# Performance work log

Hardware: AMD Instinct MI355X
Metric: run time of the kernel (lower is better)

The kernel has to match this reference:

```python
import jax, jax.numpy as jnp
import numpy as np

STRIDE = 1
PAD = 1
DIL = 1
TEMP = 30.0


def setup_inputs() -> dict:
    key = jax.random.key(0)
    ks = jax.random.split(key, 9)
    B, C, OC, H, W, E, K, HID = 16, 64, 64, 128, 128, 4, 3, 16
    return {
        "x": jax.random.normal(ks[0], (B, C, H, W), dtype=jnp.float32),
        "cw1": jax.random.normal(ks[1], (HID, C), dtype=jnp.float32) * 0.1,   # 1x1 conv C->HID
        "cw2": jax.random.normal(ks[2], (E * OC, HID), dtype=jnp.float32) * 0.1,  # 1x1 conv HID->E*OC
        "w1": jax.random.normal(ks[3], (E, OC, C, K, K), dtype=jnp.float32) * 0.05,
        "w2": jax.random.normal(ks[4], (E, OC, OC, K, K), dtype=jnp.float32) * 0.05,
        "w3": jax.random.normal(ks[5], (E, OC, OC, K, K), dtype=jnp.float32) * 0.05,
        "b1": jax.random.normal(ks[6], (E, OC), dtype=jnp.float32) * 0.05,
        "b2": jax.random.normal(ks[7], (E, OC), dtype=jnp.float32) * 0.05,
        "b3": jax.random.normal(ks[8], (E, OC), dtype=jnp.float32) * 0.05,
    }


def _batched_conv(x, w, b):
    """Per-sample conv: x (B,C,H,W), w (B,OC,C,K,K), b (B,OC).
    Equivalent to torch's groups=B trick on a flattened (1, B*C, H, W) input."""
    def one(xi, wi, bi):
        y = jax.lax.conv_general_dilated(
            xi[None], wi,
            window_strides=(STRIDE, STRIDE),
            padding=[(PAD, PAD), (PAD, PAD)],
            rhs_dilation=(DIL, DIL),
            dimension_numbers=("NCHW", "OIHW", "NCHW"),
        )[0]
        return y + bi[:, None, None]
    return jax.vmap(one)(x, w, b)


def reference(x, cw1, cw2, w1, w2, w3, b1, b2, b3):
    B = x.shape[0]
    E, OC = w1.shape[0], w1.shape[1]
    # ControlModule: global avg pool -> 1x1 conv -> relu -> 1x1 conv -> softmax over experts
    pooled = x.mean(axis=(2, 3))                       # (B, C)
    hid = jax.nn.relu(pooled @ cw1.T)                  # (B, HID)
    logits = (hid @ cw2.T).reshape(B, OC, E)           # (B, OC, E); channel layout (oc e)
    coeff = jax.nn.softmax(logits / TEMP, axis=2)      # (B, OC, E)
    # Per-sample expert-mixed weights/biases (einsum 'bce,ech->bch' in source)
    agg_w = lambda w: jnp.einsum("boe,eoikl->boikl", coeff, w)
    agg_b = lambda b: jnp.einsum("boe,eo->bo", coeff, b)
    out = _batched_conv(x, agg_w(w1), agg_b(b1))
    out = _batched_conv(out, agg_w(w2), agg_b(b2))
    out = _batched_conv(out, agg_w(w3), agg_b(b3))
    return out
```

## Files before the change

kernel.cpp:

```cpp
#include <hip/hip_runtime.h>
#include <math.h>

#define B_   16
#define C_   64
#define OC_  64
#define H_   128
#define W_   128
#define E_   4
#define HID_ 16
#define HW_  (H_ * W_)
#define TEMP_ 30.0f

#define PSTR ((size_t)B_ * HW_ * 32)

typedef float f32x4 __attribute__((ext_vector_type(4)));
typedef short s16x8 __attribute__((ext_vector_type(8)));
typedef short s16x4 __attribute__((ext_vector_type(4)));

__device__ __forceinline__ unsigned short f2bf(float f) {
    unsigned u = __float_as_uint(f);
    u = u + 0x7FFFu + ((u >> 16) & 1u);
    return (unsigned short)(u >> 16);
}
__device__ __forceinline__ float bf2f(unsigned short h) {
    return __uint_as_float(((unsigned)h) << 16);
}

__global__ void pool_kernel(const float* __restrict__ x, float* __restrict__ pooled) {
    int bc = blockIdx.x;
    const float4* xp = (const float4*)(x + (size_t)bc * HW_);
    float s = 0.f;
    for (int i = threadIdx.x; i < HW_ / 4; i += 256) {
        float4 v = xp[i];
        s += v.x + v.y + v.z + v.w;
    }
    for (int off = 32; off; off >>= 1) s += __shfl_down(s, off, 64);
    __shared__ float red[4];
    int lane = threadIdx.x & 63, wv = threadIdx.x >> 6;
    if (lane == 0) red[wv] = s;
    __syncthreads();
    if (threadIdx.x == 0)
        pooled[bc] = (red[0] + red[1] + red[2] + red[3]) * (1.0f / (float)HW_);
}

__global__ void control_kernel(const float* __restrict__ pooled,
                               const float* __restrict__ cw1,
                               const float* __restrict__ cw2,
                               const float* __restrict__ b1,
                               const float* __restrict__ b2,
                               const float* __restrict__ b3,
                               float* __restrict__ coeff,
                               float* __restrict__ ab_all) {
    int b = blockIdx.x;
    int t = threadIdx.x;
    __shared__ float pl[C_];
    __shared__ float hid[HID_];
    pl[t] = pooled[b * C_ + t];
    __syncthreads();
    if (t < HID_) {
        float a = 0.f;
        for (int c = 0; c < C_; ++c) a = fmaf(pl[c], cw1[t * C_ + c], a);
        hid[t] = fmaxf(a, 0.f);
    }
    __syncthreads();
    float l[E_];
#pragma unroll
    for (int e = 0; e < E_; ++e) {
        float a = 0.f;
#pragma unroll
        for (int h = 0; h < HID_; ++h) a = fmaf(hid[h], cw2[(t * E_ + e) * HID_ + h], a);
        l[e] = a * (1.0f / TEMP_);
    }
    float m = fmaxf(fmaxf(l[0], l[1]), fmaxf(l[2], l[3]));
    float p[E_], s = 0.f;
#pragma unroll
    for (int e = 0; e < E_; ++e) { p[e] = expf(l[e] - m); s += p[e]; }
    float inv = 1.0f / s;
#pragma unroll
    for (int e = 0; e < E_; ++e) { p[e] *= inv; coeff[(b * OC_ + t) * E_ + e] = p[e]; }
    float a1 = 0.f, a2 = 0.f, a3 = 0.f;
#pragma unroll
    for (int e = 0; e < E_; ++e) {
        a1 = fmaf(p[e], b1[e * OC_ + t], a1);
        a2 = fmaf(p[e], b2[e * OC_ + t], a2);
        a3 = fmaf(p[e], b3[e * OC_ + t], a3);
    }
    ab_all[0 * B_ * OC_ + b * OC_ + t] = a1;
    ab_all[1 * B_ * OC_ + b * OC_ + t] = a2;
    ab_all[2 * B_ * OC_ + b * OC_ + t] = a3;
}

__global__ void aggw_split(const float* __restrict__ coeff,
                           const float* __restrict__ w1,
                           const float* __restrict__ w2,
                           const float* __restrict__ w3,
                           unsigned short* __restrict__ Wh1, unsigned short* __restrict__ Wl1,
                           unsigned short* __restrict__ Wh2, unsigned short* __restrict__ Wl2,
                           unsigned short* __restrict__ Wh3, unsigned short* __restrict__ Wl3) {
    int layer = blockIdx.y;
    const float* w = (layer == 0) ? w1 : (layer == 1) ? w2 : w3;
    unsigned short* Wh = (layer == 0) ? Wh1 : (layer == 1) ? Wh2 : Wh3;
    unsigned short* Wl = (layer == 0) ? Wl1 : (layer == 1) ? Wl2 : Wl3;

    int idx = blockIdx.x * 256 + threadIdx.x;
    int c   = idx & 63;
    int r   = idx >> 6;
    int tap = r % 9;
    int r2  = r / 9;
    int oc  = r2 & 63;
    int b   = r2 >> 6;

    float s = 0.f;
#pragma unroll
    for (int e = 0; e < E_; ++e)
        s = fmaf(coeff[(b * OC_ + oc) * E_ + e],
                 w[(((size_t)e * OC_ + oc) * C_ + c) * 9 + tap], s);
    unsigned short h = f2bf(s);
    Wh[idx] = h;
    Wl[idx] = f2bf(s - bf2f(h));
}

__global__ void xcvt_kernel(const float* __restrict__ x,
                            unsigned short* __restrict__ Xs) {
    __shared__ float tr[64][65];
    const int b   = blockIdx.y;
    const int hw0 = blockIdx.x * 64;
    const int t   = threadIdx.x;
    const int l   = t & 63;
    const int wv  = t >> 6;
    const float* src = x + (size_t)b * C_ * HW_;
#pragma unroll
    for (int i = 0; i < 16; ++i) {
        int c = wv * 16 + i;
        tr[l][c] = src[(size_t)c * HW_ + hw0 + l];
    }
    __syncthreads();
#pragma unroll
    for (int i = 0; i < 2; ++i) {
        int g  = t + i * 256;
        int px = g >> 3;
        int cg = (g & 7) << 3;
        s16x8 hv, lv;
#pragma unroll
        for (int j = 0; j < 8; ++j) {
            float v = tr[px][cg + j];
            unsigned short h = f2bf(v);
            hv[j] = (short)h;
            lv[j] = (short)f2bf(v - bf2f(h));
        }
        int chunk = cg >> 5;
        int off   = cg & 31;
        size_t base = ((size_t)b * HW_ + hw0 + px) * 32 + off;
        *(s16x8*)(Xs + (size_t)(0 + chunk) * PSTR + base) = hv;
        *(s16x8*)(Xs + (size_t)(2 + chunk) * PSTR + base) = lv;
    }
}

#define NGRAN 2080
__launch_bounds__(256, 2)
__global__ void conv_mfma(const unsigned short* __restrict__ Xs,
                          const unsigned short* __restrict__ Wh,
                          const unsigned short* __restrict__ Wl,
                          const float* __restrict__ bias,
                          unsigned short* __restrict__ Ys,
                          float* __restrict__ Yf,
                          int final_layer) {
    const int bid  = blockIdx.x;
    const int wg   = (bid & 7) * 128 + (bid >> 3);
    const int b    = wg >> 6;
    const int py0  = (wg & 63) * 2;

    const int t  = threadIdx.x;
    const int l  = t & 63;
    const int wv = t >> 6;
    const int lq = l >> 4;
    const int ln = l & 15;
    const int rw = wv & 1;
    const int hx = wv >> 1;

    __shared__ __align__(16) unsigned short lds_x[NGRAN * 8];

    f32x4 acc[4][4];
#pragma unroll
    for (int o = 0; o < 4; ++o)
#pragma unroll
        for (int n = 0; n < 4; ++n)
#pragma unroll
            for (int r = 0; r < 4; ++r) acc[o][n][r] = 0.f;

    const size_t pbase = (size_t)b * HW_ * 32;
    const size_t wbase = (size_t)b * OC_ * 9 * 64;

    s16x8 stg[9];
    int   stgoff[9];

#define ISSUE(ph)                                                              \
    {                                                                          \
        const unsigned short* pl_ = Xs + (size_t)(ph) * PSTR + pbase;          \
        _Pragma("unroll")                                                      \
        for (int i = 0; i < 9; ++i) {                                          \
            int g = t + i * 256;                                               \
            if (i < 8 || t < (NGRAN - 2048)) {                                 \
                int s_lin = g & 7;                                             \
                int pr    = (g >> 3) % 65;                                     \
                int row   = (g >> 3) / 65;                                     \
                int u = s_lin >> 2, q = s_lin & 3;                             \
                int ic = 2 * pr + u - 1;                                       \
                int ir = py0 + row - 1;                                        \
                s16x8 v;                                                       \
                _Pragma("unroll")                                              \
                for (int j = 0; j < 8; ++j) v[j] = 0;                          \
                if ((unsigned)ir < (unsigned)H_ && (unsigned)ic < (unsigned)W_)\
                    v = *(const s16x8*)(pl_ + ((size_t)(ir * W_ + ic)) * 32 + q * 8); \
                stg[i] = v;                                                    \
                stgoff[i] = (((row * 65 + pr) << 3) + (s_lin ^ (pr & 7))) << 3;\
            }                                                                  \
        }                                                                      \
    }

#define WRITE_STG()                                                            \
    {                                                                          \
        _Pragma("unroll")                                                      \
        for (int i = 0; i < 9; ++i)                                            \
            if (i < 8 || t < (NGRAN - 2048))                                   \
                *(s16x8*)&lds_x[stgoff[i]] = stg[i];                           \
    }

    ISSUE(0);
    WRITE_STG();
    __syncthreads();

    for (int ph = 0; ph < 4; ++ph) {
        const int hi    = (ph < 2);
        const int cbase = (ph & 1) * 32;

        if (ph < 3) ISSUE(ph + 1);

        s16x8 Ah[2][4], Al[2][4];
#define LOADA(tp, pp)                                                          \
        {                                                                      \
            _Pragma("unroll")                                                  \
            for (int oct = 0; oct < 4; ++oct) {                                \
                size_t off = wbase + ((size_t)((oct * 16 + ln) * 9 + (tp))) * 64 \
                             + cbase + lq * 8;                                 \
                Ah[pp][oct] = *(const s16x8*)(Wh + off);                       \
                if (hi) Al[pp][oct] = *(const s16x8*)(Wl + off);               \
            }                                                                  \
        }
        LOADA(0, 0);
#pragma unroll
        for (int tap = 0; tap < 9; ++tap) {
            const int pp = tap & 1;
            if (tap < 8) LOADA(tap + 1, pp ^ 1);
            const int ky  = tap / 3;
            const int kx  = tap % 3;
            const int row = rw + ky;
            s16x8 Bv[4];
#pragma unroll
            for (int nt = 0; nt < 4; ++nt) {
                int col  = hx * 64 + nt * 16 + ln + kx;
                int pr   = col >> 1, u = col & 1;
                int slot = (u * 4 + lq) ^ (pr & 7);
                Bv[nt] = *(const s16x8*)&lds_x[(((row * 65 + pr) << 3) + slot) << 3];
            }
#pragma unroll
            for (int oct = 0; oct < 4; ++oct)
#pragma unroll
                for (int nt = 0; nt < 4; ++nt)
                    acc[oct][nt] = __builtin_amdgcn_mfma_f32_16x16x32_bf16(
                        Ah[pp][oct], Bv[nt], acc[oct][nt], 0, 0, 0);
            if (hi) {
#pragma unroll
                for (int oct = 0; oct < 4; ++oct)
#pragma unroll
                    for (int nt = 0; nt < 4; ++nt)
                        acc[oct][nt] = __builtin_amdgcn_mfma_f32_16x16x32_bf16(
                            Al[pp][oct], Bv[nt], acc[oct][nt], 0, 0, 0);
            }
        }
#undef LOADA

        __syncthreads();
        if (ph < 3) {
            WRITE_STG();
            __syncthreads();
        }
    }

    float bia[4][4];
#pragma unroll
    for (int oct = 0; oct < 4; ++oct)
#pragma unroll
        for (int r = 0; r < 4; ++r)
            bia[oct][r] = bias[b * OC_ + oct * 16 + lq * 4 + r];

    const int orow = py0 + rw;
    if (!final_layer) {
#pragma unroll
        for (int oct = 0; oct < 4; ++oct)
#pragma unroll
            for (int nt = 0; nt < 4; ++nt) {
                int px = hx * 64 + nt * 16 + ln;
                size_t pxl = (size_t)b * HW_ + orow * W_ + px;
                int oc0   = oct * 16 + lq * 4;
                int chunk = oc0 >> 5;
                int off   = oc0 & 31;
                s16x4 hv, lv;
#pragma unroll
                for (int r = 0; r < 4; ++r) {
                    float v = acc[oct][nt][r] + bia[oct][r];
                    unsigned short h = f2bf(v);
                    hv[r] = (short)h;
                    lv[r] = (short)f2bf(v - bf2f(h));
                }
                *(s16x4*)(Ys + (size_t)(0 + chunk) * PSTR + pxl * 32 + off) = hv;
                *(s16x4*)(Ys + (size_t)(2 + chunk) * PSTR + pxl * 32 + off) = lv;
            }
    } else {
#pragma unroll
        for (int oct = 0; oct < 4; ++oct)
#pragma unroll
            for (int nt = 0; nt < 4; ++nt) {
                int px = hx * 64 + nt * 16 + ln;
#pragma unroll
                for (int r = 0; r < 4; ++r) {
                    int oc = oct * 16 + lq * 4 + r;
                    Yf[((size_t)(b * OC_ + oc)) * HW_ + orow * W_ + px] =
                        acc[oct][nt][r] + bia[oct][r];
                }
            }
    }
#undef ISSUE
#undef WRITE_STG
}

extern "C" void kernel_launch(void* const* d_in, const int* in_sizes, int n_in,
                              void* d_out, int out_size, void* d_ws, size_t ws_size,
                              hipStream_t stream) {
    const float* x   = (const float*)d_in[0];
    const float* cw1 = (const float*)d_in[1];
    const float* cw2 = (const float*)d_in[2];
    const float* w1  = (const float*)d_in[3];
    const float* w2  = (const float*)d_in[4];
    const float* w3  = (const float*)d_in[5];
    const float* b1  = (const float*)d_in[6];
    const float* b2  = (const float*)d_in[7];
    const float* b3  = (const float*)d_in[8];

    char* ws = (char*)d_ws;
    float* pooled = (float*)(ws + 0);
    float* coeff  = (float*)(ws + 4096);
    float* ab_all = (float*)(ws + 20480);
    const size_t WSZ = (size_t)B_ * OC_ * 9 * 64 * 2;
    unsigned short* Wh1 = (unsigned short*)(ws + 32768);
    unsigned short* Wl1 = (unsigned short*)(ws + 32768 + 1 * WSZ);
    unsigned short* Wh2 = (unsigned short*)(ws + 32768 + 2 * WSZ);
    unsigned short* Wl2 = (unsigned short*)(ws + 32768 + 3 * WSZ);
    unsigned short* Wh3 = (unsigned short*)(ws + 32768 + 4 * WSZ);
    unsigned short* Wl3 = (unsigned short*)(ws + 32768 + 5 * WSZ);
    const size_t SOFF = 32768 + 6 * WSZ;
    const size_t SSZ  = 4 * PSTR * 2;
    unsigned short* S0 = (unsigned short*)(ws + SOFF);
    unsigned short* S1 = (unsigned short*)(ws + SOFF + SSZ);

    float* ab1 = ab_all;
    float* ab2 = ab_all + B_ * OC_;
    float* ab3 = ab_all + 2 * B_ * OC_;

    pool_kernel<<<B_ * C_, 256, 0, stream>>>(x, pooled);
    control_kernel<<<B_, 64, 0, stream>>>(pooled, cw1, cw2, b1, b2, b3, coeff, ab_all);
    {
        dim3 g(2304, 3);
        aggw_split<<<g, 256, 0, stream>>>(coeff, w1, w2, w3,
                                          Wh1, Wl1, Wh2, Wl2, Wh3, Wl3);
    }
    {
        dim3 g(HW_ / 64, B_);
        xcvt_kernel<<<g, 256, 0, stream>>>(x, S0);
    }
    conv_mfma<<<1024, 256, 0, stream>>>(S0, Wh1, Wl1, ab1, S1, nullptr, 0);
    conv_mfma<<<1024, 256, 0, stream>>>(S1, Wh2, Wl2, ab2, S0, nullptr, 0);
    conv_mfma<<<1024, 256, 0, stream>>>(S0, Wh3, Wl3, ab3, nullptr, (float*)d_out, 1);
}
```

Measured before the change: 541.7 us.

## Double-buffer LDS input tiles and split output channels across 8 waves

```diff
diff --git a/kernel.cpp b/kernel.cpp
--- a/kernel.cpp
+++ b/kernel.cpp
@@ -157,7 +157,7 @@
 }
 
 #define NGRAN 2080
-__launch_bounds__(256, 2)
+__launch_bounds__(512, 4)
 __global__ void conv_mfma(const unsigned short* __restrict__ Xs,
                           const unsigned short* __restrict__ Wh,
                           const unsigned short* __restrict__ Wl,
@@ -176,13 +176,14 @@
     const int lq = l >> 4;
     const int ln = l & 15;
     const int rw = wv & 1;
-    const int hx = wv >> 1;
-
-    __shared__ __align__(16) unsigned short lds_x[NGRAN * 8];
-
-    f32x4 acc[4][4];
-#pragma unroll
-    for (int o = 0; o < 4; ++o)
+    const int hx = (wv >> 1) & 1;
+    const int oh = wv >> 2;
+
+    __shared__ __align__(16) unsigned short lds_x[2][NGRAN * 8];
+
+    f32x4 acc[2][4];
+#pragma unroll
+    for (int o = 0; o < 2; ++o)
 #pragma unroll
         for (int n = 0; n < 4; ++n)
 #pragma unroll
@@ -191,16 +192,15 @@
     const size_t pbase = (size_t)b * HW_ * 32;
     const size_t wbase = (size_t)b * OC_ * 9 * 64;
 
-    s16x8 stg[9];
-    int   stgoff[9];
+    s16x8 stg[5];
 
 #define ISSUE(ph)                                                              \
     {                                                                          \
         const unsigned short* pl_ = Xs + (size_t)(ph) * PSTR + pbase;          \
         _Pragma("unroll")                                                      \
-        for (int i = 0; i < 9; ++i) {                                          \
-            int g = t + i * 256;                                               \
-            if (i < 8 || t < (NGRAN - 2048)) {                                 \
+        for (int i = 0; i < 5; ++i) {                                          \
+            if (i < 4 || t < (NGRAN - 2048)) {                                 \
+                int g = t + i * 512;                                           \
                 int s_lin = g & 7;                                             \
                 int pr    = (g >> 3) % 65;                                     \
                 int row   = (g >> 3) / 65;                                     \
@@ -213,38 +213,47 @@
                 if ((unsigned)ir < (unsigned)H_ && (unsigned)ic < (unsigned)W_)\
                     v = *(const s16x8*)(pl_ + ((size_t)(ir * W_ + ic)) * 32 + q * 8); \
                 stg[i] = v;                                                    \
-                stgoff[i] = (((row * 65 + pr) << 3) + (s_lin ^ (pr & 7))) << 3;\
             }                                                                  \
         }                                                                      \
     }
 
-#define WRITE_STG()                                                            \
+#define WRITE_STG(bf)                                                          \
     {                                                                          \
         _Pragma("unroll")                                                      \
-        for (int i = 0; i < 9; ++i)                                            \
-            if (i < 8 || t < (NGRAN - 2048))                                   \
-                *(s16x8*)&lds_x[stgoff[i]] = stg[i];                           \
+        for (int i = 0; i < 5; ++i) {                                          \
+            if (i < 4 || t < (NGRAN - 2048)) {                                 \
+                int g = t + i * 512;                                           \
+                int s_lin = g & 7;                                             \
+                int pr    = (g >> 3) % 65;                                     \
+                int row   = (g >> 3) / 65;                                     \
+                int off   = (((row * 65 + pr) << 3) + (s_lin ^ (pr & 7))) << 3;\
+                *(s16x8*)&lds_x[bf][off] = stg[i];                             \
+            }                                                                  \
+        }                                                                      \
     }
 
     ISSUE(0);
-    WRITE_STG();
-    __syncthreads();
-
-    for (int ph = 0; ph < 4; ++ph) {
-        const int hi    = (ph < 2);
-        const int cbase = (ph & 1) * 32;
-
-        if (ph < 3) ISSUE(ph + 1);
-
-        s16x8 Ah[2][4], Al[2][4];
+    WRITE_STG(0);
+    ISSUE(1);
+
+#pragma unroll
+    for (int p = 0; p < 4; ++p) {
+        const int hi    = (p < 2);
+        const int cbase = (p & 1) * 32;
+
+        __syncthreads();
+        if (p < 3) WRITE_STG((p + 1) & 1);
+        if (p < 2) ISSUE(p + 2);
+
+        s16x8 Ah[2][2], Al[2][2];
 #define LOADA(tp, pp)                                                          \
         {                                                                      \
             _Pragma("unroll")                                                  \
-            for (int oct = 0; oct < 4; ++oct) {                                \
-                size_t off = wbase + ((size_t)((oct * 16 + ln) * 9 + (tp))) * 64 \
+            for (int o = 0; o < 2; ++o) {                                      \
+                size_t off = wbase + ((size_t)(((oh * 2 + o) * 16 + ln) * 9 + (tp))) * 64 \
                              + cbase + lq * 8;                                 \
-                Ah[pp][oct] = *(const s16x8*)(Wh + off);                       \
-                if (hi) Al[pp][oct] = *(const s16x8*)(Wl + off);               \
+                Ah[pp][o] = *(const s16x8*)(Wh + off);                         \
+                if (hi) Al[pp][o] = *(const s16x8*)(Wl + off);                 \
             }                                                                  \
         }
         LOADA(0, 0);
@@ -261,54 +270,48 @@
                 int col  = hx * 64 + nt * 16 + ln + kx;
                 int pr   = col >> 1, u = col & 1;
                 int slot = (u * 4 + lq) ^ (pr & 7);
-                Bv[nt] = *(const s16x8*)&lds_x[(((row * 65 + pr) << 3) + slot) << 3];
+                Bv[nt] = *(const s16x8*)&lds_x[p & 1][(((row * 65 + pr) << 3) + slot) << 3];
             }
 #pragma unroll
-            for (int oct = 0; oct < 4; ++oct)
+            for (int o = 0; o < 2; ++o)
 #pragma unroll
                 for (int nt = 0; nt < 4; ++nt)
-                    acc[oct][nt] = __builtin_amdgcn_mfma_f32_16x16x32_bf16(
-                        Ah[pp][oct], Bv[nt], acc[oct][nt], 0, 0, 0);
+                    acc[o][nt] = __builtin_amdgcn_mfma_f32_16x16x32_bf16(
+                        Ah[pp][o], Bv[nt], acc[o][nt], 0, 0, 0);
             if (hi) {
 #pragma unroll
-                for (int oct = 0; oct < 4; ++oct)
+                for (int o = 0; o < 2; ++o)
 #pragma unroll
                     for (int nt = 0; nt < 4; ++nt)
-                        acc[oct][nt] = __builtin_amdgcn_mfma_f32_16x16x32_bf16(
-                            Al[pp][oct], Bv[nt], acc[oct][nt], 0, 0, 0);
+                        acc[o][nt] = __builtin_amdgcn_mfma_f32_16x16x32_bf16(
+                            Al[pp][o], Bv[nt], acc[o][nt], 0, 0, 0);
             }
         }
 #undef LOADA
-
-        __syncthreads();
-        if (ph < 3) {
-            WRITE_STG();
-            __syncthreads();
-        }
-    }
-
-    float bia[4][4];
-#pragma unroll
-    for (int oct = 0; oct < 4; ++oct)
+    }
+
+    float bia[2][4];
+#pragma unroll
+    for (int o = 0; o < 2; ++o)
 #pragma unroll
         for (int r = 0; r < 4; ++r)
-            bia[oct][r] = bias[b * OC_ + oct * 16 + lq * 4 + r];
+            bia[o][r] = bias[b * OC_ + (oh * 2 + o) * 16 + lq * 4 + r];
 
     const int orow = py0 + rw;
     if (!final_layer) {
 #pragma unroll
-        for (int oct = 0; oct < 4; ++oct)
+        for (int o = 0; o < 2; ++o)
 #pragma unroll
             for (int nt = 0; nt < 4; ++nt) {
                 int px = hx * 64 + nt * 16 + ln;
                 size_t pxl = (size_t)b * HW_ + orow * W_ + px;
-                int oc0   = oct * 16 + lq * 4;
+                int oc0   = (oh * 2 + o) * 16 + lq * 4;
                 int chunk = oc0 >> 5;
                 int off   = oc0 & 31;
                 s16x4 hv, lv;
 #pragma unroll
                 for (int r = 0; r < 4; ++r) {
-                    float v = acc[oct][nt][r] + bia[oct][r];
+                    float v = acc[o][nt][r] + bia[o][r];
                     unsigned short h = f2bf(v);
                     hv[r] = (short)h;
                     lv[r] = (short)f2bf(v - bf2f(h));
@@ -318,15 +321,15 @@
             }
     } else {
 #pragma unroll
-        for (int oct = 0; oct < 4; ++oct)
+        for (int o = 0; o < 2; ++o)
 #pragma unroll
             for (int nt = 0; nt < 4; ++nt) {
                 int px = hx * 64 + nt * 16 + ln;
 #pragma unroll
                 for (int r = 0; r < 4; ++r) {
-                    int oc = oct * 16 + lq * 4 + r;
+                    int oc = (oh * 2 + o) * 16 + lq * 4 + r;
                     Yf[((size_t)(b * OC_ + oc)) * HW_ + orow * W_ + px] =
-                        acc[oct][nt][r] + bia[oct][r];
+                        acc[o][nt][r] + bia[o][r];
                 }
             }
     }
@@ -378,7 +381,7 @@
         dim3 g(HW_ / 64, B_);
         xcvt_kernel<<<g, 256, 0, stream>>>(x, S0);
     }
-    conv_mfma<<<1024, 256, 0, stream>>>(S0, Wh1, Wl1, ab1, S1, nullptr, 0);
-    conv_mfma<<<1024, 256, 0, stream>>>(S1, Wh2, Wl2, ab2, S0, nullptr, 0);
-    conv_mfma<<<1024, 256, 0, stream>>>(S0, Wh3, Wl3, ab3, nullptr, (float*)d_out, 1);
-}
+    conv_mfma<<<1024, 512, 0, stream>>>(S0, Wh1, Wl1, ab1, S1, nullptr, 0);
+    conv_mfma<<<1024, 512, 0, stream>>>(S1, Wh2, Wl2, ab2, S0, nullptr, 0);
+    conv_mfma<<<1024, 512, 0, stream>>>(S0, Wh3, Wl3, ab3, nullptr, (float*)d_out, 1);
+}
```

After: 727.0 us. +34.2%, slower.

## Restructure conv into two channel halves with hi/lo planes and 512-thread blocks

Applied to the files above, without the earlier changes.

```diff
diff --git a/kernel.cpp b/kernel.cpp
--- a/kernel.cpp
+++ b/kernel.cpp
@@ -156,8 +156,8 @@
     }
 }
 
-#define NGRAN 2080
-__launch_bounds__(256, 2)
+#define NG 4160
+__launch_bounds__(512, 1)
 __global__ void conv_mfma(const unsigned short* __restrict__ Xs,
                           const unsigned short* __restrict__ Wh,
                           const unsigned short* __restrict__ Wl,
@@ -176,15 +176,16 @@
     const int lq = l >> 4;
     const int ln = l & 15;
     const int rw = wv & 1;
-    const int hx = wv >> 1;
-
-    __shared__ __align__(16) unsigned short lds_x[NGRAN * 8];
-
-    f32x4 acc[4][4];
+    const int qx = wv >> 1;
+
+    __shared__ __align__(16) unsigned short ldsA[NG * 8];
+    __shared__ __align__(16) unsigned short ldsB[NG * 8];
+
+    f32x4 acc[4][2];
 #pragma unroll
     for (int o = 0; o < 4; ++o)
 #pragma unroll
-        for (int n = 0; n < 4; ++n)
+        for (int n = 0; n < 2; ++n)
 #pragma unroll
             for (int r = 0; r < 4; ++r) acc[o][n][r] = 0.f;
 
@@ -192,100 +193,105 @@
     const size_t wbase = (size_t)b * OC_ * 9 * 64;
 
     s16x8 stg[9];
-    int   stgoff[9];
-
-#define ISSUE(ph)                                                              \
+
+#define ISSUE(ch)                                                              \
     {                                                                          \
-        const unsigned short* pl_ = Xs + (size_t)(ph) * PSTR + pbase;          \
         _Pragma("unroll")                                                      \
         for (int i = 0; i < 9; ++i) {                                          \
-            int g = t + i * 256;                                               \
-            if (i < 8 || t < (NGRAN - 2048)) {                                 \
-                int s_lin = g & 7;                                             \
-                int pr    = (g >> 3) % 65;                                     \
-                int row   = (g >> 3) / 65;                                     \
-                int u = s_lin >> 2, q = s_lin & 3;                             \
+            if (i < 8 || t < (NG - 4096)) {                                    \
+                int g    = t + i * 512;                                        \
+                int row  = g / 1040;                                           \
+                int rem  = g - row * 1040;                                     \
+                int pr   = rem >> 4;                                           \
+                int slot = rem & 15;                                           \
+                int s_lin = slot ^ (pr & 7);                                   \
+                int k = s_lin >> 3, u = (s_lin >> 2) & 1, q = s_lin & 3;       \
+                int ir = py0 + row - 1;                                        \
                 int ic = 2 * pr + u - 1;                                       \
-                int ir = py0 + row - 1;                                        \
                 s16x8 v;                                                       \
                 _Pragma("unroll")                                              \
                 for (int j = 0; j < 8; ++j) v[j] = 0;                          \
                 if ((unsigned)ir < (unsigned)H_ && (unsigned)ic < (unsigned)W_)\
-                    v = *(const s16x8*)(pl_ + ((size_t)(ir * W_ + ic)) * 32 + q * 8); \
+                    v = *(const s16x8*)(Xs + (size_t)(k * 2 + (ch)) * PSTR + pbase \
+                        + ((size_t)(ir * W_ + ic)) * 32 + q * 8);              \
                 stg[i] = v;                                                    \
-                stgoff[i] = (((row * 65 + pr) << 3) + (s_lin ^ (pr & 7))) << 3;\
             }                                                                  \
         }                                                                      \
     }
 
-#define WRITE_STG()                                                            \
+#define WRITE_STG(BUF)                                                         \
     {                                                                          \
         _Pragma("unroll")                                                      \
         for (int i = 0; i < 9; ++i)                                            \
-            if (i < 8 || t < (NGRAN - 2048))                                   \
-                *(s16x8*)&lds_x[stgoff[i]] = stg[i];                           \
+            if (i < 8 || t < (NG - 4096))                                      \
+                *(s16x8*)&(BUF)[(t + i * 512) * 8] = stg[i];                   \
+    }
+
+#define TAPS(BUF, CBASE)                                                       \
+    {                                                                          \
+        s16x8 Ah[2][4], Al[2][4];                                              \
+        _Pragma("unroll")                                                      \
+        for (int oct = 0; oct < 4; ++oct) {                                    \
+            size_t woff = wbase + ((size_t)((oct * 16 + ln) * 9)) * 64         \
+                          + (CBASE) + lq * 8;                                  \
+            Ah[0][oct] = *(const s16x8*)(Wh + woff);                           \
+            Al[0][oct] = *(const s16x8*)(Wl + woff);                           \
+        }                                                                      \
+        _Pragma("unroll")                                                      \
+        for (int tap = 0; tap < 9; ++tap) {                                    \
+            const int pp = tap & 1;                                            \
+            if (tap < 8) {                                                     \
+                _Pragma("unroll")                                              \
+                for (int oct = 0; oct < 4; ++oct) {                            \
+                    size_t woff = wbase + ((size_t)((oct * 16 + ln) * 9 + tap + 1)) * 64 \
+                                  + (CBASE) + lq * 8;                          \
+                    Ah[pp ^ 1][oct] = *(const s16x8*)(Wh + woff);              \
+                    Al[pp ^ 1][oct] = *(const s16x8*)(Wl + woff);              \
+                }                                                              \
+            }                                                                  \
+            const int ky  = tap / 3;                                           \
+            const int kx  = tap - ky * 3;                                       \
+            const int row = rw + ky;                                           \
+            s16x8 Bh[2], Bl[2];                                                \
+            _Pragma("unroll")                                                  \
+            for (int nt = 0; nt < 2; ++nt) {                                   \
+                int col = qx * 32 + nt * 16 + ln + kx;                         \
+                int pr  = col >> 1, u = col & 1;                               \
+                int bse = (row * 65 + pr) << 4;                                \
+                Bh[nt] = *(const s16x8*)&(BUF)[(bse + ((u * 4 + lq) ^ (pr & 7))) << 3];      \
+                Bl[nt] = *(const s16x8*)&(BUF)[(bse + ((8 + u * 4 + lq) ^ (pr & 7))) << 3];  \
+            }                                                                  \
+            _Pragma("unroll")                                                  \
+            for (int oct = 0; oct < 4; ++oct)                                  \
+                _Pragma("unroll")                                              \
+                for (int nt = 0; nt < 2; ++nt)                                 \
+                    acc[oct][nt] = __builtin_amdgcn_mfma_f32_16x16x32_bf16(    \
+                        Ah[pp][oct], Bh[nt], acc[oct][nt], 0, 0, 0);           \
+            _Pragma("unroll")                                                  \
+            for (int oct = 0; oct < 4; ++oct)                                  \
+                _Pragma("unroll")                                              \
+                for (int nt = 0; nt < 2; ++nt)                                 \
+                    acc[oct][nt] = __builtin_amdgcn_mfma_f32_16x16x32_bf16(    \
+                        Al[pp][oct], Bh[nt], acc[oct][nt], 0, 0, 0);           \
+            _Pragma("unroll")                                                  \
+            for (int oct = 0; oct < 4; ++oct)                                  \
+                _Pragma("unroll")                                              \
+                for (int nt = 0; nt < 2; ++nt)                                 \
+                    acc[oct][nt] = __builtin_amdgcn_mfma_f32_16x16x32_bf16(    \
+                        Ah[pp][oct], Bl[nt], acc[oct][nt], 0, 0, 0);           \
+        }                                                                      \
     }
 
     ISSUE(0);
-    WRITE_STG();
-    __syncthreads();
-
-    for (int ph = 0; ph < 4; ++ph) {
-        const int hi    = (ph < 2);
-        const int cbase = (ph & 1) * 32;
-
-        if (ph < 3) ISSUE(ph + 1);
-
-        s16x8 Ah[2][4], Al[2][4];
-#define LOADA(tp, pp)                                                          \
-        {                                                                      \
-            _Pragma("unroll")                                                  \
-            for (int oct = 0; oct < 4; ++oct) {                                \
-                size_t off = wbase + ((size_t)((oct * 16 + ln) * 9 + (tp))) * 64 \
-                             + cbase + lq * 8;                                 \
-                Ah[pp][oct] = *(const s16x8*)(Wh + off);                       \
-                if (hi) Al[pp][oct] = *(const s16x8*)(Wl + off);               \
-            }                                                                  \
-        }
-        LOADA(0, 0);
-#pragma unroll
-        for (int tap = 0; tap < 9; ++tap) {
-            const int pp = tap & 1;
-            if (tap < 8) LOADA(tap + 1, pp ^ 1);
-            const int ky  = tap / 3;
-            const int kx  = tap % 3;
-            const int row = rw + ky;
-            s16x8 Bv[4];
-#pragma unroll
-            for (int nt = 0; nt < 4; ++nt) {
-                int col  = hx * 64 + nt * 16 + ln + kx;
-                int pr   = col >> 1, u = col & 1;
-                int slot = (u * 4 + lq) ^ (pr & 7);
-                Bv[nt] = *(const s16x8*)&lds_x[(((row * 65 + pr) << 3) + slot) << 3];
-            }
-#pragma unroll
-            for (int oct = 0; oct < 4; ++oct)
-#pragma unroll
-                for (int nt = 0; nt < 4; ++nt)
-                    acc[oct][nt] = __builtin_amdgcn_mfma_f32_16x16x32_bf16(
-                        Ah[pp][oct], Bv[nt], acc[oct][nt], 0, 0, 0);
-            if (hi) {
-#pragma unroll
-                for (int oct = 0; oct < 4; ++oct)
-#pragma unroll
-                    for (int nt = 0; nt < 4; ++nt)
-                        acc[oct][nt] = __builtin_amdgcn_mfma_f32_16x16x32_bf16(
-                            Al[pp][oct], Bv[nt], acc[oct][nt], 0, 0, 0);
-            }
-        }
-#undef LOADA
-
-        __syncthreads();
-        if (ph < 3) {
-            WRITE_STG();
-            __syncthreads();
-        }
-    }
+    WRITE_STG(ldsA);
+    ISSUE(1);
+    __syncthreads();
+
+    TAPS(ldsA, 0);
+    WRITE_STG(ldsB);
+    __syncthreads();
+
+    TAPS(ldsB, 32);
 
     float bia[4][4];
 #pragma unroll
@@ -299,8 +305,8 @@
 #pragma unroll
         for (int oct = 0; oct < 4; ++oct)
 #pragma unroll
-            for (int nt = 0; nt < 4; ++nt) {
-                int px = hx * 64 + nt * 16 + ln;
+            for (int nt = 0; nt < 2; ++nt) {
+                int px = qx * 32 + nt * 16 + ln;
                 size_t pxl = (size_t)b * HW_ + orow * W_ + px;
                 int oc0   = oct * 16 + lq * 4;
                 int chunk = oc0 >> 5;
@@ -320,8 +326,8 @@
 #pragma unroll
         for (int oct = 0; oct < 4; ++oct)
 #pragma unroll
-            for (int nt = 0; nt < 4; ++nt) {
-                int px = hx * 64 + nt * 16 + ln;
+            for (int nt = 0; nt < 2; ++nt) {
+                int px = qx * 32 + nt * 16 + ln;
 #pragma unroll
                 for (int r = 0; r < 4; ++r) {
                     int oc = oct * 16 + lq * 4 + r;
@@ -332,6 +338,7 @@
     }
 #undef ISSUE
 #undef WRITE_STG
+#undef TAPS
 }
 
 extern "C" void kernel_launch(void* const* d_in, const int* in_sizes, int n_in,
@@ -378,7 +385,7 @@
         dim3 g(HW_ / 64, B_);
         xcvt_kernel<<<g, 256, 0, stream>>>(x, S0);
     }
-    conv_mfma<<<1024, 256, 0, stream>>>(S0, Wh1, Wl1, ab1, S1, nullptr, 0);
-    conv_mfma<<<1024, 256, 0, stream>>>(S1, Wh2, Wl2, ab2, S0, nullptr, 0);
-    conv_mfma<<<1024, 256, 0, stream>>>(S0, Wh3, Wl3, ab3, nullptr, (float*)d_out, 1);
-}
+    conv_mfma<<<1024, 512, 0, stream>>>(S0, Wh1, Wl1, ab1, S1, nullptr, 0);
+    conv_mfma<<<1024, 512, 0, stream>>>(S1, Wh2, Wl2, ab2, S0, nullptr, 0);
+    conv_mfma<<<1024, 512, 0, stream>>>(S0, Wh3, Wl3, ab3, nullptr, (float*)d_out, 1);
+}
```

New measurement: 618.8 us. +14.2%, slower.
